# Performance work log

Measured on AMD Instinct MI355X. Metric: run time of the kernel, lower is better.

## Reference

```python
import jax, jax.numpy as jnp
import numpy as np

B, S = 1, 1863
D_MODEL, H = 1024, 16
HD = D_MODEL // H  # 64
MAX_X, MAX_Y, MAX_Z = 32, 32, 8
BASE = 10000.0
MAX_DXY, MAX_DZ = 30, 8
N_PAIRS = HD // 2
PX = N_PAIRS // 3  # 10
PY = N_PAIRS // 3  # 10
PZ = N_PAIRS - PX - PY  # 12


def _rotate_half(x):
    # (x0,x1,x2,x3,...) -> (-x1,x0,-x3,x2,...)
    x1 = x[..., ::2]
    x2 = x[..., 1::2]
    return jnp.stack((-x2, x1), axis=-1).reshape(x.shape)


def _rope_tables(max_pos, dim):
    inv = 1.0 / (BASE ** (np.arange(0, dim, 2, dtype=np.float32) / dim))
    f = np.outer(np.arange(max_pos, dtype=np.float32), inv)
    return jnp.asarray(np.cos(f)), jnp.asarray(np.sin(f))


def setup_inputs() -> dict:
    key = jax.random.key(0)
    ks = jax.random.split(key, 8)
    x = jax.random.normal(ks[0], (B, S, D_MODEL), dtype=jnp.float32)
    Wqkv = jax.random.normal(ks[1], (3 * D_MODEL, D_MODEL), dtype=jnp.float32) * 0.02
    Wout = jax.random.normal(ks[2], (D_MODEL, D_MODEL), dtype=jnp.float32) * 0.02
    bias_x = jax.random.normal(ks[3], (2 * MAX_DXY + 1, H), dtype=jnp.float32) * 0.02
    bias_y = jax.random.normal(ks[4], (2 * MAX_DXY + 1, H), dtype=jnp.float32) * 0.02
    bias_z = jax.random.normal(ks[5], (2 * MAX_DZ + 1, H), dtype=jnp.float32) * 0.02
    pos_xyz = jax.random.randint(ks[6], (B, S, 3), 0, 32, dtype=jnp.int32)
    return {"x": x, "Wqkv": Wqkv, "Wout": Wout, "bias_x": bias_x,
            "bias_y": bias_y, "bias_z": bias_z, "pos_xyz": pos_xyz}


def _apply_rope3d(q, k, pos_xyz):
    cx, sx = _rope_tables(MAX_X, 2 * PX)
    cy, sy = _rope_tables(MAX_Y, 2 * PY)
    cz, sz = _rope_tables(MAX_Z, 2 * PZ)
    xp = jnp.clip(pos_xyz[..., 0], 0, MAX_X - 1)
    yp = jnp.clip(pos_xyz[..., 1], 0, MAX_Y - 1)
    zp = jnp.clip(pos_xyz[..., 2], 0, MAX_Z - 1)
    # [B,S,head_dim] after repeat-interleave(2) per axis, then concat
    cos = jnp.concatenate([jnp.repeat(cx[xp], 2, axis=-1),
                           jnp.repeat(cy[yp], 2, axis=-1),
                           jnp.repeat(cz[zp], 2, axis=-1)], axis=-1)[:, :, None, :]
    sin = jnp.concatenate([jnp.repeat(sx[xp], 2, axis=-1),
                           jnp.repeat(sy[yp], 2, axis=-1),
                           jnp.repeat(sz[zp], 2, axis=-1)], axis=-1)[:, :, None, :]
    q_rot = q * cos + _rotate_half(q) * sin
    k_rot = k * cos + _rotate_half(k) * sin
    return q_rot, k_rot


def reference(x, Wqkv, Wout, bias_x, bias_y, bias_z, pos_xyz):
    b, s, _ = x.shape
    qkv = x @ Wqkv.T  # [B,S,3*D]
    q, k, v = jnp.split(qkv, 3, axis=-1)
    q = q.reshape(b, s, H, HD)
    k = k.reshape(b, s, H, HD)
    v = v.reshape(b, s, H, HD)
    q, k = _apply_rope3d(q, k, pos_xyz)
    scores = jnp.einsum('bqhd,bkhd->bhqk', q, k) * (HD ** -0.5)
    # 3D relative position bias
    px_, py_, pz_ = pos_xyz[..., 0], pos_xyz[..., 1], pos_xyz[..., 2]
    dx = jnp.clip(px_[:, :, None] - px_[:, None, :], -MAX_DXY, MAX_DXY) + MAX_DXY
    dy = jnp.clip(py_[:, :, None] - py_[:, None, :], -MAX_DXY, MAX_DXY) + MAX_DXY
    dz = jnp.clip(pz_[:, :, None] - pz_[:, None, :], -MAX_DZ, MAX_DZ) + MAX_DZ
    bias = (bias_x[dx] + bias_y[dy] + bias_z[dz]).transpose(0, 3, 1, 2)  # [B,H,S,S]
    scores = scores + bias
    causal = jnp.tril(jnp.ones((s, s), dtype=bool))
    scores = jnp.where(causal, scores, -jnp.inf)
    attn = jax.nn.softmax(scores, axis=-1)
    out = jnp.einsum('bhqk,bkhd->bqhd', attn, v).reshape(b, s, D_MODEL)
    return out @ Wout.T
```

## Files before the change

### kernel.cpp

```cpp
#include <hip/hip_runtime.h>

typedef __bf16 bf16;
typedef __bf16 bf16x2 __attribute__((ext_vector_type(2)));
typedef __bf16 bf16x4 __attribute__((ext_vector_type(4)));
typedef __bf16 bf16x8 __attribute__((ext_vector_type(8)));
typedef float  f32x4  __attribute__((ext_vector_type(4)));
typedef short  short4v __attribute__((ext_vector_type(4)));

#define S_LEN 1863
#define S_PAD 1920
#define DM 1024
#define NH 16
#define HDIM 64
#define AUGD 160
#define KA_STR 168
#define QKV_STRIDE 3072
#define NQT128 15
#define CHUNK 4
#define MAXC 8
#define NQMULTI 13
#define NCHUNK_HEAD 64

#define MFMA_BF16 __builtin_amdgcn_mfma_f32_16x16x32_bf16
#define MFMA_BF16_K16 __builtin_amdgcn_mfma_f32_16x16x16bf16_1k

__constant__ int QT_BASE[15] = {0, 1, 2, 4, 6, 9, 12, 16, 20, 25, 30, 36, 42, 49, 56};

__device__ __forceinline__ void dma16(const bf16* g, bf16* l) {
  __builtin_amdgcn_global_load_lds(
      (const __attribute__((address_space(1))) unsigned int*)g,
      (__attribute__((address_space(3))) unsigned int*)l, 16, 0, 0);
}

__device__ __forceinline__ short4v as_s4(bf16x4 v) {
  return __builtin_bit_cast(short4v, v);
}

__global__ void cvt3(const float* __restrict__ a, bf16* __restrict__ oa, int na4,
                     const float* __restrict__ b, bf16* __restrict__ ob, int nb4,
                     const float* __restrict__ c, bf16* __restrict__ oc, int nc4) {
  int j = blockIdx.x * blockDim.x + threadIdx.x;
  const float* s; bf16* d;
  if (j < na4) { s = a; d = oa; }
  else {
    j -= na4;
    if (j < nb4) { s = b; d = ob; }
    else { j -= nb4; if (j >= nc4) return; s = c; d = oc; }
  }
  float4 v = ((const float4*)s)[j];
  bf16x4 o;
  o[0] = (bf16)v.x; o[1] = (bf16)v.y; o[2] = (bf16)v.z; o[3] = (bf16)v.w;
  ((bf16x4*)d)[j] = o;
}

template <typename T>
__global__ __launch_bounds__(256) void gemm_bt(const bf16* __restrict__ A,
                                               const bf16* __restrict__ B,
                                               T* __restrict__ C,
                                               int M, int N, int K) {
  __shared__ bf16 As[128][32];
  __shared__ bf16 Bs[64][32];
  const int t = threadIdx.x;
  const int w = t >> 6, l = t & 63;
  const int quad = l >> 4, l16 = l & 15;
  const int wm = w >> 1, wn = w & 1;
  const int bm = blockIdx.y * 128, bn = blockIdx.x * 64;
  const int lr = l >> 2;
  const int lc = (l & 3) * 8;

  f32x4 acc[4][2];
#pragma unroll
  for (int mi = 0; mi < 4; ++mi)
#pragma unroll
    for (int ni = 0; ni < 2; ++ni) acc[mi][ni] = 0;

  for (int k0 = 0; k0 < K; k0 += 32) {
    __syncthreads();
#pragma unroll
    for (int p = 0; p < 2; ++p) {
      const int seg = 2 * w + p;
      const int row = seg * 16 + lr;
      dma16(&A[(size_t)min(bm + row, M - 1) * K + k0 + lc], &As[seg * 16][0]);
    }
    dma16(&B[(size_t)(bn + w * 16 + lr) * K + k0 + lc], &Bs[w * 16][0]);
    __syncthreads();

    bf16x8 af[4], bfr[2];
#pragma unroll
    for (int mi = 0; mi < 4; ++mi) af[mi]  = *(bf16x8*)&As[wm * 64 + mi * 16 + l16][quad * 8];
#pragma unroll
    for (int ni = 0; ni < 2; ++ni) bfr[ni] = *(bf16x8*)&Bs[wn * 32 + ni * 16 + l16][quad * 8];
#pragma unroll
    for (int mi = 0; mi < 4; ++mi)
#pragma unroll
      for (int ni = 0; ni < 2; ++ni)
        acc[mi][ni] = MFMA_BF16(af[mi], bfr[ni], acc[mi][ni], 0, 0, 0);
  }

#pragma unroll
  for (int mi = 0; mi < 4; ++mi)
#pragma unroll
    for (int r = 0; r < 4; ++r) {
      int m = bm + wm * 64 + mi * 16 + quad * 4 + r;
      if (m < M) {
#pragma unroll
        for (int ni = 0; ni < 2; ++ni)
          C[(size_t)m * N + bn + wn * 32 + ni * 16 + l16] = (T)acc[mi][ni][r];
      }
    }
}

__global__ __launch_bounds__(256) void gemm_bt64(const bf16* __restrict__ A,
                                                 const bf16* __restrict__ B,
                                                 float* __restrict__ C,
                                                 int M, int N, int K) {
  __shared__ bf16 As[64][32];
  __shared__ bf16 Bs[64][32];
  const int t = threadIdx.x;
  const int w = t >> 6, l = t & 63;
  const int quad = l >> 4, l16 = l & 15;
  const int wm = w >> 1, wn = w & 1;
  const int bm = blockIdx.y * 64, bn = blockIdx.x * 64;
  const int lr = l >> 2;
  const int lc = (l & 3) * 8;

  f32x4 acc[2][2];
#pragma unroll
  for (int mi = 0; mi < 2; ++mi)
#pragma unroll
    for (int ni = 0; ni < 2; ++ni) acc[mi][ni] = 0;

  for (int k0 = 0; k0 < K; k0 += 32) {
    __syncthreads();
    dma16(&A[(size_t)min(bm + w * 16 + lr, M - 1) * K + k0 + lc], &As[w * 16][0]);
    dma16(&B[(size_t)(bn + w * 16 + lr) * K + k0 + lc], &Bs[w * 16][0]);
    __syncthreads();

    bf16x8 af[2], bfr[2];
#pragma unroll
    for (int mi = 0; mi < 2; ++mi) af[mi]  = *(bf16x8*)&As[wm * 32 + mi * 16 + l16][quad * 8];
#pragma unroll
    for (int ni = 0; ni < 2; ++ni) bfr[ni] = *(bf16x8*)&Bs[wn * 32 + ni * 16 + l16][quad * 8];
#pragma unroll
    for (int mi = 0; mi < 2; ++mi)
#pragma unroll
      for (int ni = 0; ni < 2; ++ni)
        acc[mi][ni] = MFMA_BF16(af[mi], bfr[ni], acc[mi][ni], 0, 0, 0);
  }

#pragma unroll
  for (int mi = 0; mi < 2; ++mi)
#pragma unroll
    for (int r = 0; r < 4; ++r) {
      int m = bm + wm * 32 + mi * 16 + quad * 4 + r;
      if (m < M) {
#pragma unroll
        for (int ni = 0; ni < 2; ++ni)
          C[(size_t)m * N + bn + wn * 32 + ni * 16 + l16] = acc[mi][ni][r];
      }
    }
}

__global__ __launch_bounds__(256) void pack_all(const bf16* __restrict__ qkv,
                                                const int* __restrict__ pos,
                                                const float* __restrict__ bxg,
                                                const float* __restrict__ byg,
                                                const float* __restrict__ bzg,
                                                bf16* __restrict__ Qa,
                                                bf16* __restrict__ Ka,
                                                bf16* __restrict__ Vt) {
  const int st = blockIdx.x, h = blockIdx.y;
  const int t = threadIdx.x;
  __shared__ float bxs[61], bys[61], bzs[17];
  __shared__ float vtile[64][68];

  if (t < 61) { bxs[t] = bxg[t * NH + h]; bys[t] = byg[t * NH + h]; }
  if (t < 17) bzs[t] = bzg[t * NH + h];

  for (int i = t; i < 1024; i += 256) {
    int row = i >> 4, c4 = (i & 15) * 4;
    int sg = min(st * 64 + row, S_LEN - 1);
    bf16x4 v = *(const bf16x4*)&qkv[(size_t)sg * QKV_STRIDE + 2 * DM + h * HDIM + c4];
    *(float4*)&vtile[row][c4] = make_float4((float)v[0], (float)v[1], (float)v[2], (float)v[3]);
  }
  __syncthreads();

  for (int i = t; i < 2048; i += 256) {
    const int sl = i >> 5, sub = i & 31;
    const int s = st * 64 + sl;
    const int sc = min(s, S_LEN - 1);
    const int px = pos[sc * 3 + 0], py = pos[sc * 3 + 1], pz = pos[sc * 3 + 2];
    int j, P, pp;
    if (sub < 10)      { j = sub;      P = 10; pp = min(max(px, 0), 31); }
    else if (sub < 20) { j = sub - 10; P = 10; pp = min(max(py, 0), 31); }
    else               { j = sub - 20; P = 12; pp = min(max(pz, 0), 7);  }
    const float inv = __expf(-(float)j / (float)P * 9.210340371976184f);
    const float ang = (float)pp * inv;
    float sn, cs;
    __sincosf(ang, &sn, &cs);
    const size_t base = (size_t)sc * QKV_STRIDE + h * HDIM + 2 * sub;
    bf16x2 q2 = *(const bf16x2*)&qkv[base];
    bf16x2 k2 = *(const bf16x2*)&qkv[base + DM];
    float q0 = (float)q2[0], q1 = (float)q2[1];
    float k0 = (float)k2[0], k1 = (float)k2[1];
    const size_t qb = ((size_t)h * S_PAD + s) * AUGD;
    const size_t kb = ((size_t)h * S_PAD + s) * KA_STR;
    bf16x2 oq, ok;
    oq[0] = (bf16)((q0 * cs - q1 * sn) * 0.125f);
    oq[1] = (bf16)((q1 * cs + q0 * sn) * 0.125f);
    ok[0] = (bf16)(k0 * cs - k1 * sn);
    ok[1] = (bf16)(k1 * cs + k0 * sn);
    *(bf16x2*)&Qa[qb + 2 * sub] = oq;
    *(bf16x2*)&Ka[kb + 2 * sub] = ok;

    const int ix = min(max(px - sub, -30), 30) + 30;
    const int iy = min(max(py - sub, -30), 30) + 30;
    const int iz = min(max(pz - sub, -8), 8) + 8;
    Qa[qb + 64 + sub]  = (bf16)bxs[ix];
    Qa[qb + 96 + sub]  = (bf16)bys[iy];
    Qa[qb + 128 + sub] = (bf16)bzs[iz];
    Ka[kb + 64 + sub]  = (bf16)(sub == px ? 1.0f : 0.0f);
    Ka[kb + 96 + sub]  = (bf16)(sub == py ? 1.0f : 0.0f);
    Ka[kb + 128 + sub] = (bf16)(sub == pz ? 1.0f : 0.0f);
  }

  for (int i = t; i < 1024; i += 256) {
    int d = i >> 4, s4 = (i & 15) * 4;
    bf16x4 o;
    o[0] = (bf16)vtile[s4 + 0][d];
    o[1] = (bf16)vtile[s4 + 1][d];
    o[2] = (bf16)vtile[s4 + 2][d];
    o[3] = (bf16)vtile[s4 + 3][d];
    *(bf16x4*)&Vt[((size_t)h * HDIM + d) * S_PAD + st * 64 + s4] = o;
  }
}

__global__ __launch_bounds__(256) void attn_split(const bf16* __restrict__ Qa,
                                                  const bf16* __restrict__ Ka,
                                                  const bf16* __restrict__ Vt,
                                                  bf16* __restrict__ outb,
                                                  bf16* __restrict__ Opart,
                                                  float* __restrict__ lpart) {
  const int b = blockIdx.x;
  const int h = b & 15;
  const int id = 63 - (b >> 4);
  int qt = 14;
  while (QT_BASE[qt] > id) --qt;
  const int c = id - QT_BASE[qt];
  const int chain = 2 * qt + 2;
  const int k0 = c * CHUNK;
  const int kend = min(k0 + CHUNK, chain);

  const int t = threadIdx.x, w = t >> 6, l = t & 63;
  const int quad = l >> 4, l16 = l & 15;

  __shared__ bf16 Ks[64][KA_STR];
  __shared__ bf16 Vs[64][72];

  bf16x8 bq[2][5];
  int igm[2];
#pragma unroll
  for (int mi = 0; mi < 2; ++mi) {
    const int qrow = qt * 128 + w * 32 + mi * 16 + l16;
    igm[mi] = qrow;
    const bf16* qp = &Qa[((size_t)h * S_PAD + qrow) * AUGD + quad * 8];
#pragma unroll
    for (int sg = 0; sg < 5; ++sg) bq[mi][sg] = *(const bf16x8*)(qp + sg * 32);
  }

  f32x4 O[2][4];
#pragma unroll
  for (int mi = 0; mi < 2; ++mi)
#pragma unroll
    for (int di = 0; di < 4; ++di) O[mi][di] = 0;
  float lacc[2] = {0.f, 0.f};

  bf16* KsF = &Ks[0][0];

  for (int kt = k0; kt < kend; ++kt) {
    __syncthreads();
    {
      const bf16* gtile = &Ka[((size_t)h * S_PAD + kt * 64) * KA_STR];
#pragma unroll
      for (int seg = 0; seg < 6; ++seg) {
        int sidx = w + seg * 4;
        if (sidx < 21) dma16(gtile + sidx * 512 + l * 8, KsF + sidx * 512);
      }
    }
    for (int i = t; i < 512; i += 256) {
      int row = i >> 3, c8 = (i & 7) * 8;
      *(bf16x8*)&Vs[row][c8] =
          *(const bf16x8*)&Vt[((size_t)h * HDIM + row) * S_PAD + kt * 64 + c8];
    }
    __syncthreads();

    f32x4 sf[2][4];
#pragma unroll
    for (int ni = 0; ni < 4; ++ni) {
      bf16x8 ak[5];
      const bf16* kp = &Ks[ni * 16 + l16][quad * 8];
#pragma unroll
      for (int sg = 0; sg < 5; ++sg) ak[sg] = *(const bf16x8*)(kp + sg * 32);
#pragma unroll
      for (int mi = 0; mi < 2; ++mi) {
        f32x4 z = {0.f, 0.f, 0.f, 0.f};
#pragma unroll
        for (int sg = 0; sg < 5; ++sg) z = MFMA_BF16(ak[sg], bq[mi][sg], z, 0, 0, 0);
        sf[mi][ni] = z;
      }
    }

    short4v pf[2][4];
#pragma unroll
    for (int mi = 0; mi < 2; ++mi)
#pragma unroll
      for (int ni = 0; ni < 4; ++ni) {
        bf16x4 pb;
#pragma unroll
        for (int r = 0; r < 4; ++r) {
          const int key = kt * 64 + ni * 16 + quad * 4 + r;
          float p = __expf(sf[mi][ni][r]);
          if (key > igm[mi]) p = 0.f;
          lacc[mi] += p;
          pb[r] = (bf16)p;
        }
        pf[mi][ni] = as_s4(pb);
      }

#pragma unroll
    for (int g = 0; g < 4; ++g)
#pragma unroll
      for (int di = 0; di < 4; ++di) {
        short4v vf = as_s4(*(const bf16x4*)&Vs[di * 16 + l16][g * 16 + quad * 4]);
#pragma unroll
        for (int mi = 0; mi < 2; ++mi)
          O[mi][di] = MFMA_BF16_K16(vf, pf[mi][g], O[mi][di], 0, 0, 0);
      }
  }

#pragma unroll
  for (int mi = 0; mi < 2; ++mi) {
    float v = lacc[mi];
    v += __shfl_xor(v, 16);
    v += __shfl_xor(v, 32);
    lacc[mi] = v;
  }

  if (k0 == 0 && kend == chain) {
#pragma unroll
    for (int mi = 0; mi < 2; ++mi) {
      const int qrow = igm[mi];
      if (qrow < S_LEN) {
        const float inv = 1.0f / lacc[mi];
#pragma unroll
        for (int di = 0; di < 4; ++di) {
          bf16x4 o;
#pragma unroll
          for (int r = 0; r < 4; ++r) o[r] = (bf16)(O[mi][di][r] * inv);
          *(bf16x4*)&outb[(size_t)qrow * DM + h * HDIM + di * 16 + quad * 4] = o;
        }
      }
    }
  } else {
    bf16* ob = Opart + (((size_t)h * NQMULTI + (qt - 2)) * MAXC + c) * 8192;
#pragma unroll
    for (int mi = 0; mi < 2; ++mi) {
      const int row32 = w * 32 + mi * 16 + l16;
#pragma unroll
      for (int di = 0; di < 4; ++di) {
        bf16x4 o;
#pragma unroll
        for (int r = 0; r < 4; ++r) o[r] = (bf16)O[mi][di][r];
        *(bf16x4*)&ob[row32 * 64 + di * 16 + quad * 4] = o;
      }
    }
    if (quad == 0) {
      float* lb = lpart + (((size_t)h * NQMULTI + (qt - 2)) * MAXC + c) * 128;
#pragma unroll
      for (int mi = 0; mi < 2; ++mi) lb[w * 32 + mi * 16 + l16] = lacc[mi];
    }
  }
}

__global__ __launch_bounds__(256) void attn_combine(const bf16* __restrict__ Opart,
                                                    const float* __restrict__ lpart,
                                                    bf16* __restrict__ outb) {
  const int qt = blockIdx.x + 2;
  const int h = blockIdx.y;
  const int t = threadIdx.x;
  const int row = t >> 1, half = t & 1;
  const int nchunk = (2 * qt + 5) >> 2;
  float acc[32];
#pragma unroll
  for (int j = 0; j < 32; ++j) acc[j] = 0.f;
  float lsum = 0.f;
  const size_t pb = ((size_t)h * NQMULTI + (qt - 2)) * MAXC;
  for (int cc = 0; cc < nchunk; ++cc) {
    const bf16x8* p8 = (const bf16x8*)(Opart + (pb + cc) * 8192 + row * 64 + half * 32);
#pragma unroll
    for (int j = 0; j < 4; ++j) {
      bf16x8 v = p8[j];
#pragma unroll
      for (int e = 0; e < 8; ++e) acc[j * 8 + e] += (float)v[e];
    }
    lsum += lpart[(pb + cc) * 128 + row];
  }
  const int s = qt * 128 + row;
  if (s < S_LEN) {
    const float inv = 1.0f / lsum;
    bf16* op = outb + (size_t)s * DM + h * HDIM + half * 32;
#pragma unroll
    for (int j = 0; j < 8; ++j) {
      bf16x4 o;
      o[0] = (bf16)(acc[j * 4 + 0] * inv);
      o[1] = (bf16)(acc[j * 4 + 1] * inv);
      o[2] = (bf16)(acc[j * 4 + 2] * inv);
      o[3] = (bf16)(acc[j * 4 + 3] * inv);
      *(bf16x4*)&op[j * 4] = o;
    }
  }
}

extern "C" void kernel_launch(void* const* d_in, const int* in_sizes, int n_in,
                              void* d_out, int out_size, void* d_ws, size_t ws_size,
                              hipStream_t stream) {
  const float* x    = (const float*)d_in[0];
  const float* Wqkv = (const float*)d_in[1];
  const float* Wout = (const float*)d_in[2];
  const float* bx   = (const float*)d_in[3];
  const float* by   = (const float*)d_in[4];
  const float* bz   = (const float*)d_in[5];
  const int*   pos  = (const int*)d_in[6];
  float* out = (float*)d_out;

  char* ws = (char*)d_ws;
  bf16* Opart = (bf16*)ws;
  bf16* xb    = (bf16*)ws;
  bf16* wqkvb = xb + (size_t)S_LEN * DM;
  bf16* qkvb  = wqkvb + (size_t)QKV_STRIDE * DM;
  ws += (size_t)NH * NQMULTI * MAXC * 8192 * 2;
  bf16* woutb = (bf16*)ws;   ws += (size_t)DM * DM * 2;
  bf16* Qaug  = (bf16*)ws;   ws += (size_t)NH * S_PAD * AUGD * 2;
  bf16* Kaug  = (bf16*)ws;   ws += (size_t)NH * S_PAD * KA_STR * 2;
  bf16* Vtb   = (bf16*)ws;   ws += (size_t)NH * S_PAD * HDIM * 2;
  bf16* attnb = (bf16*)ws;   ws += (size_t)S_LEN * DM * 2;
  float* lpart = (float*)ws; ws += (size_t)NH * NQMULTI * MAXC * 128 * 4;

  const int na4 = S_LEN * DM / 4, nb4 = QKV_STRIDE * DM / 4, nc4 = DM * DM / 4;
  const int ntot = na4 + nb4 + nc4;
  cvt3<<<dim3((ntot + 255) / 256), 256, 0, stream>>>(x, xb, na4, Wqkv, wqkvb, nb4, Wout, woutb, nc4);
  gemm_bt<bf16><<<dim3(QKV_STRIDE / 64, NQT128), 256, 0, stream>>>(
      xb, wqkvb, qkvb, S_LEN, QKV_STRIDE, DM);
  pack_all<<<dim3(S_PAD / 64, NH), 256, 0, stream>>>(qkvb, pos, bx, by, bz, Qaug, Kaug, Vtb);
  attn_split<<<dim3(NH * NCHUNK_HEAD), 256, 0, stream>>>(Qaug, Kaug, Vtb, attnb, Opart, lpart);
  attn_combine<<<dim3(NQMULTI, NH), 256, 0, stream>>>(Opart, lpart, attnb);
  gemm_bt64<<<dim3(DM / 64, (S_LEN + 63) / 64), 256, 0, stream>>>(
      attnb, woutb, out, S_LEN, DM, DM);
}
```

Baseline: 166.7 us.

## Widen QKV GEMM tile to 128x128 and DMA tiled V into LDS

The QKV projection GEMM now computes 128x128 output tiles per block instead of 128x64, which doubles register accumulators and improves operand reuse but halves the grid to 24x15 blocks. V^T is stored as padded per-tile 64x72 chunks, so the attention kernel can load V straight into LDS with the same async global-to-LDS DMA used for K. This replaces the register-staged V copy and lets both loads overlap. The padded stride presumably matches the Vs shared array layout.

```diff
diff --git a/kernel.cpp b/kernel.cpp
--- a/kernel.cpp
+++ b/kernel.cpp
@@ -14,8 +14,10 @@
 #define HDIM 64
 #define AUGD 160
 #define KA_STR 168
+#define VT_TILE 4608
 #define QKV_STRIDE 3072
 #define NQT128 15
+#define NT64 30
 #define CHUNK 4
 #define MAXC 8
 #define NQMULTI 13
@@ -54,46 +56,45 @@
 }
 
 template <typename T>
-__global__ __launch_bounds__(256) void gemm_bt(const bf16* __restrict__ A,
-                                               const bf16* __restrict__ B,
-                                               T* __restrict__ C,
-                                               int M, int N, int K) {
+__global__ __launch_bounds__(256) void gemm_bt128(const bf16* __restrict__ A,
+                                                  const bf16* __restrict__ B,
+                                                  T* __restrict__ C,
+                                                  int M, int N, int K) {
   __shared__ bf16 As[128][32];
-  __shared__ bf16 Bs[64][32];
+  __shared__ bf16 Bs[128][32];
   const int t = threadIdx.x;
   const int w = t >> 6, l = t & 63;
   const int quad = l >> 4, l16 = l & 15;
   const int wm = w >> 1, wn = w & 1;
-  const int bm = blockIdx.y * 128, bn = blockIdx.x * 64;
+  const int bm = blockIdx.y * 128, bn = blockIdx.x * 128;
   const int lr = l >> 2;
   const int lc = (l & 3) * 8;
 
-  f32x4 acc[4][2];
+  f32x4 acc[4][4];
 #pragma unroll
   for (int mi = 0; mi < 4; ++mi)
 #pragma unroll
-    for (int ni = 0; ni < 2; ++ni) acc[mi][ni] = 0;
+    for (int ni = 0; ni < 4; ++ni) acc[mi][ni] = 0;
 
   for (int k0 = 0; k0 < K; k0 += 32) {
     __syncthreads();
 #pragma unroll
     for (int p = 0; p < 2; ++p) {
       const int seg = 2 * w + p;
-      const int row = seg * 16 + lr;
-      dma16(&A[(size_t)min(bm + row, M - 1) * K + k0 + lc], &As[seg * 16][0]);
-    }
-    dma16(&B[(size_t)(bn + w * 16 + lr) * K + k0 + lc], &Bs[w * 16][0]);
-    __syncthreads();
-
-    bf16x8 af[4], bfr[2];
+      dma16(&A[(size_t)min(bm + seg * 16 + lr, M - 1) * K + k0 + lc], &As[seg * 16][0]);
+      dma16(&B[(size_t)(bn + seg * 16 + lr) * K + k0 + lc], &Bs[seg * 16][0]);
+    }
+    __syncthreads();
+
+    bf16x8 af[4], bfr[4];
 #pragma unroll
     for (int mi = 0; mi < 4; ++mi) af[mi]  = *(bf16x8*)&As[wm * 64 + mi * 16 + l16][quad * 8];
 #pragma unroll
-    for (int ni = 0; ni < 2; ++ni) bfr[ni] = *(bf16x8*)&Bs[wn * 32 + ni * 16 + l16][quad * 8];
+    for (int ni = 0; ni < 4; ++ni) bfr[ni] = *(bf16x8*)&Bs[wn * 64 + ni * 16 + l16][quad * 8];
 #pragma unroll
     for (int mi = 0; mi < 4; ++mi)
 #pragma unroll
-      for (int ni = 0; ni < 2; ++ni)
+      for (int ni = 0; ni < 4; ++ni)
         acc[mi][ni] = MFMA_BF16(af[mi], bfr[ni], acc[mi][ni], 0, 0, 0);
   }
 
@@ -104,8 +105,8 @@
       int m = bm + wm * 64 + mi * 16 + quad * 4 + r;
       if (m < M) {
 #pragma unroll
-        for (int ni = 0; ni < 2; ++ni)
-          C[(size_t)m * N + bn + wn * 32 + ni * 16 + l16] = (T)acc[mi][ni][r];
+        for (int ni = 0; ni < 4; ++ni)
+          C[(size_t)m * N + bn + wn * 64 + ni * 16 + l16] = (T)acc[mi][ni][r];
       }
     }
 }
@@ -224,6 +225,7 @@
     Ka[kb + 128 + sub] = (bf16)(sub == pz ? 1.0f : 0.0f);
   }
 
+  bf16* vout = Vt + (size_t)(h * NT64 + st) * VT_TILE;
   for (int i = t; i < 1024; i += 256) {
     int d = i >> 4, s4 = (i & 15) * 4;
     bf16x4 o;
@@ -231,7 +233,7 @@
     o[1] = (bf16)vtile[s4 + 1][d];
     o[2] = (bf16)vtile[s4 + 2][d];
     o[3] = (bf16)vtile[s4 + 3][d];
-    *(bf16x4*)&Vt[((size_t)h * HDIM + d) * S_PAD + st * 64 + s4] = o;
+    *(bf16x4*)&vout[d * 72 + s4] = o;
   }
 }
 
@@ -276,21 +278,19 @@
   float lacc[2] = {0.f, 0.f};
 
   bf16* KsF = &Ks[0][0];
+  bf16* VsF = &Vs[0][0];
 
   for (int kt = k0; kt < kend; ++kt) {
     __syncthreads();
     {
-      const bf16* gtile = &Ka[((size_t)h * S_PAD + kt * 64) * KA_STR];
-#pragma unroll
-      for (int seg = 0; seg < 6; ++seg) {
-        int sidx = w + seg * 4;
-        if (sidx < 21) dma16(gtile + sidx * 512 + l * 8, KsF + sidx * 512);
-      }
-    }
-    for (int i = t; i < 512; i += 256) {
-      int row = i >> 3, c8 = (i & 7) * 8;
-      *(bf16x8*)&Vs[row][c8] =
-          *(const bf16x8*)&Vt[((size_t)h * HDIM + row) * S_PAD + kt * 64 + c8];
+      const bf16* gk = &Ka[((size_t)h * S_PAD + kt * 64) * KA_STR];
+      const bf16* gv = &Vt[(size_t)(h * NT64 + kt) * VT_TILE];
+#pragma unroll
+      for (int it = 0; it < 8; ++it) {
+        const int sidx = w + it * 4;
+        if (sidx < 21)      dma16(gk + sidx * 512 + l * 8, KsF + sidx * 512);
+        else if (sidx < 30) dma16(gv + (sidx - 21) * 512 + l * 8, VsF + (sidx - 21) * 512);
+      }
     }
     __syncthreads();
 
@@ -442,16 +442,16 @@
   bf16* woutb = (bf16*)ws;   ws += (size_t)DM * DM * 2;
   bf16* Qaug  = (bf16*)ws;   ws += (size_t)NH * S_PAD * AUGD * 2;
   bf16* Kaug  = (bf16*)ws;   ws += (size_t)NH * S_PAD * KA_STR * 2;
-  bf16* Vtb   = (bf16*)ws;   ws += (size_t)NH * S_PAD * HDIM * 2;
+  bf16* Vtb   = (bf16*)ws;   ws += (size_t)NH * NT64 * VT_TILE * 2;
   bf16* attnb = (bf16*)ws;   ws += (size_t)S_LEN * DM * 2;
   float* lpart = (float*)ws; ws += (size_t)NH * NQMULTI * MAXC * 128 * 4;
 
   const int na4 = S_LEN * DM / 4, nb4 = QKV_STRIDE * DM / 4, nc4 = DM * DM / 4;
   const int ntot = na4 + nb4 + nc4;
   cvt3<<<dim3((ntot + 255) / 256), 256, 0, stream>>>(x, xb, na4, Wqkv, wqkvb, nb4, Wout, woutb, nc4);
-  gemm_bt<bf16><<<dim3(QKV_STRIDE / 64, NQT128), 256, 0, stream>>>(
+  gemm_bt128<bf16><<<dim3(QKV_STRIDE / 128, NQT128), 256, 0, stream>>>(
       xb, wqkvb, qkvb, S_LEN, QKV_STRIDE, DM);
-  pack_all<<<dim3(S_PAD / 64, NH), 256, 0, stream>>>(qkvb, pos, bx, by, bz, Qaug, Kaug, Vtb);
+  pack_all<<<dim3(NT64, NH), 256, 0, stream>>>(qkvb, pos, bx, by, bz, Qaug, Kaug, Vtb);
   attn_split<<<dim3(NH * NCHUNK_HEAD), 256, 0, stream>>>(Qaug, Kaug, Vtb, attnb, Opart, lpart);
   attn_combine<<<dim3(NQMULTI, NH), 256, 0, stream>>>(Opart, lpart, attnb);
   gemm_bt64<<<dim3(DM / 64, (S_LEN + 63) / 64), 256, 0, stream>>>(
```

Result: no change. 167.5 us (+0.5%).
